# Optimization experiments

Measured on AMD Instinct MI355X. Metric: run time of the kernel, lower is better.

## Reference

```python
import jax, jax.numpy as jnp
import numpy as np

B, S, H, NH, G = 2, 2048, 2048, 16, 2
HD = H // NH          # head_dim = 128
NKV = NH // G         # kv heads = 8
EPS = 1e-6


def setup_inputs() -> dict:
    key = jax.random.key(0)
    ks = jax.random.split(key, 5)
    sc = 0.02
    return {
        "x": jax.random.normal(ks[0], (B, S, H), jnp.float32),
        "wq": jax.random.normal(ks[1], (H, H), jnp.float32) * sc,
        "wk": jax.random.normal(ks[2], (H, H // G), jnp.float32) * sc,
        "wv": jax.random.normal(ks[3], (H, H // G), jnp.float32) * sc,
        "wo": jax.random.normal(ks[4], (H, H), jnp.float32) * sc,
        "rms_w": jnp.ones((HD,), jnp.float32),
        "token_positions": jnp.arange(S, dtype=jnp.int32),
    }


def _rmsnorm(x, w):
    # x: (b, s, HD, n_heads); normalize over the head_dim axis (axis 2)
    ms = jnp.mean(x * x, axis=2, keepdims=True)
    return x * jax.lax.rsqrt(ms + EPS) * w[None, None, :, None]


def _rope(x, pos):
    # x: (b, s, HD, n); interleaved-pair rotation along HD, base 10000
    half = HD // 2
    inv_freq = 1.0 / (10000.0 ** (jnp.arange(half, dtype=jnp.float32) * 2.0 / HD))
    ang = pos.astype(jnp.float32)[:, None] * inv_freq[None, :]   # (s, HD/2)
    cos = jnp.cos(ang)[None, :, :, None]
    sin = jnp.sin(ang)[None, :, :, None]
    x1 = x[:, :, 0::2, :]
    x2 = x[:, :, 1::2, :]
    r1 = x1 * cos - x2 * sin
    r2 = x1 * sin + x2 * cos
    return jnp.stack([r1, r2], axis=3).reshape(x.shape)


def reference(x, wq, wk, wv, wo, rms_w, token_positions):
    b, s, _ = x.shape
    # projections, split hidden as (head_dim, n_heads) exactly like the torch .view
    q = (x @ wq).reshape(b, s, HD, NH)
    k = (x @ wk).reshape(b, s, HD, NKV)
    v = (x @ wv).reshape(b, s, HD, NKV)
    # per-head RMSNorm (over head_dim) then RoPE on Q and K
    q = _rope(_rmsnorm(q, rms_w), token_positions)
    k = _rope(_rmsnorm(k, rms_w), token_positions)
    # grouped-query attention: group G query heads per kv head
    q5 = q.reshape(b, s, HD, NKV, G)
    scores = jnp.einsum('bsdkg,btdk->bkgst', q5, k)          # (b,NKV,G,s,s)
    mask = jnp.triu(jnp.ones((s, s), bool), 1)               # causal
    scores = jnp.where(mask[None, None, None], -jnp.inf, scores)
    attn = jax.nn.softmax(scores / jnp.sqrt(jnp.float32(HD)), axis=-1)
    ctx = jnp.einsum('bkgst,btdk->bkgsd', attn, v)           # (b,NKV,G,s,HD)
    ctx = ctx.reshape(b, NH, s, HD).transpose(0, 2, 1, 3).reshape(b, s, H)
    return ctx @ wo
```

## Files before the change

kernel.cpp:

```cpp
#include <hip/hip_runtime.h>
#include <hip/hip_bf16.h>
#include <stdint.h>

typedef unsigned short u16;
typedef uint32_t u32;
typedef __attribute__((ext_vector_type(8))) short s8v;
typedef __attribute__((ext_vector_type(4))) float f4v;
typedef __attribute__((ext_vector_type(4))) unsigned int u4v;

#define SQ   2048
#define HDIM 2048
#define HD_  128
#define NH_  16
#define NKV_ 8

__device__ __forceinline__ u16 f2b(float f) {
  uint32_t u = __builtin_bit_cast(uint32_t, f);
  u += 0x7fffu + ((u >> 16) & 1u);
  return (u16)(u >> 16);
}
__device__ __forceinline__ float b2f(u16 v) {
  uint32_t u = ((uint32_t)v) << 16;
  return __builtin_bit_cast(float, u);
}
__device__ __forceinline__ u32 cvtpk(float lo, float hi) {
  u32 r;
  asm("v_cvt_pk_bf16_f32 %0, %1, %2" : "=v"(r) : "v"(lo), "v"(hi));
  return r;
}

__global__ __launch_bounds__(256) void k_prep(const float* __restrict__ x,
                                              const float* __restrict__ wq,
                                              const float* __restrict__ wk,
                                              const float* __restrict__ wv,
                                              const float* __restrict__ wo,
                                              u16* __restrict__ xb,
                                              u16* __restrict__ wqt,
                                              u16* __restrict__ wkt,
                                              u16* __restrict__ wvt,
                                              u16* __restrict__ wot) {
  const int z = blockIdx.z;
  if (z == 4) {
    size_t i = ((size_t)(blockIdx.y * 64 + blockIdx.x) * 256 + threadIdx.x) * 2;
#pragma unroll
    for (int j = 0; j < 2; j++) {
      f4v v = *(const f4v*)(x + (i + j) * 4);
      union { u16 s[4]; uint64_t u; } o;
      o.s[0] = f2b(v[0]); o.s[1] = f2b(v[1]); o.s[2] = f2b(v[2]); o.s[3] = f2b(v[3]);
      *(uint64_t*)(xb + (i + j) * 4) = o.u;
    }
    return;
  }
  const float* in = (z == 0) ? wq : (z == 1) ? wk : (z == 2) ? wv : wo;
  u16* out = (z == 0) ? wqt : (z == 1) ? wkt : (z == 2) ? wvt : wot;
  const int cols = (z == 1 || z == 2) ? 1024 : 2048;
  int c0 = blockIdx.x * 32, r0 = blockIdx.y * 32;
  if (c0 >= cols) return;
  __shared__ float tile[32][33];
  int tx = threadIdx.x & 31, ty = threadIdx.x >> 5;
#pragma unroll
  for (int i = 0; i < 32; i += 8)
    tile[ty + i][tx] = in[(size_t)(r0 + ty + i) * cols + c0 + tx];
  __syncthreads();
#pragma unroll
  for (int i = 0; i < 32; i += 8)
    out[(size_t)(c0 + ty + i) * 2048 + r0 + tx] = f2b(tile[tx][ty + i]);
}

template <int BN, int F32OUT>
__global__ __launch_bounds__(512, 2) void k_gemm256(const u16* __restrict__ A,
                                                    const u16* __restrict__ Bt,
                                                    void* __restrict__ C,
                                                    int M, int N, int K) {
  constexpr int NB = BN / 64;
  constexpr int NF = BN / 64;
  __shared__ __align__(16) u16 Al[2][256 * 64];
  __shared__ __align__(16) u16 Bl[2][BN * 64];
  const int tid = threadIdx.x;
  const int lane = tid & 63, wid = tid >> 6;
  const int wm = wid >> 2, wn = wid & 3;
  const int l15 = lane & 15, l4 = lane >> 4;
  const int m0 = blockIdx.y * 256, n0 = blockIdx.x * BN;
  auto* A3 = (__attribute__((address_space(3))) char*)&Al[0][0];
  auto* B3 = (__attribute__((address_space(3))) char*)&Bl[0][0];
  int srow[4], soff[4];
#pragma unroll
  for (int j = 0; j < 4; j++) {
    int slot = j * 8192 + tid * 16;
    srow[j] = slot >> 7;
    soff[j] = (((slot >> 4) & 7) ^ (srow[j] & 7)) * 16;
  }
  int xk2[2];
#pragma unroll
  for (int ks = 0; ks < 2; ks++) xk2[ks] = (((ks * 4 + l4) ^ (l15 & 7)) << 4);

#define STAGEAB(buf, k0s)                                                         \
  do {                                                                            \
    _Pragma("unroll")                                                             \
    for (int j = 0; j < 4; j++) {                                                 \
      const char* gA = (const char*)(A + (size_t)(m0 + srow[j]) * K + (k0s)) + soff[j]; \
      __builtin_amdgcn_global_load_lds(                                           \
          (const __attribute__((address_space(1))) void*)gA,                      \
          (__attribute__((address_space(3))) void*)(A3 + (buf) * 32768 + j * 8192 + tid * 16), \
          16, 0, 0);                                                              \
    }                                                                             \
    _Pragma("unroll")                                                             \
    for (int j = 0; j < NB; j++) {                                                \
      const char* gB = (const char*)(Bt + (size_t)(n0 + srow[j]) * K + (k0s)) + soff[j]; \
      __builtin_amdgcn_global_load_lds(                                           \
          (const __attribute__((address_space(1))) void*)gB,                      \
          (__attribute__((address_space(3))) void*)(B3 + (buf) * (BN * 128) + j * 8192 + tid * 16), \
          16, 0, 0);                                                              \
    }                                                                             \
  } while (0)

  f4v acc[8][NF] = {};
  STAGEAB(0, 0);
  STAGEAB(1, 64);
  const int nK = K >> 6;
  for (int t = 0; t < nK; t++) {
    if (t == nK - 1)  asm volatile("s_waitcnt vmcnt(0)" ::: "memory");
    else if (NB == 4) asm volatile("s_waitcnt vmcnt(8)" ::: "memory");
    else              asm volatile("s_waitcnt vmcnt(6)" ::: "memory");
    __builtin_amdgcn_s_barrier();
    __builtin_amdgcn_sched_barrier(0);
    const char* Ab = (const char*)&Al[0][0] + (t & 1) * 32768;
    const char* Bb = (const char*)&Bl[0][0] + (t & 1) * (BN * 128);
#pragma unroll
    for (int qm = 0; qm < 2; qm++)
#pragma unroll
      for (int qn = 0; qn < 2; qn++) {
        s8v af[4][2], bf2[NF / 2][2];
#pragma unroll
        for (int i2 = 0; i2 < 4; i2++) {
          int row = wm * 128 + (qm * 4 + i2) * 16 + l15;
#pragma unroll
          for (int ks = 0; ks < 2; ks++)
            af[i2][ks] = *(const s8v*)(Ab + row * 128 + xk2[ks]);
        }
#pragma unroll
        for (int j2 = 0; j2 < NF / 2; j2++) {
          int row = wn * (NF * 16) + (qn * (NF / 2) + j2) * 16 + l15;
#pragma unroll
          for (int ks = 0; ks < 2; ks++)
            bf2[j2][ks] = *(const s8v*)(Bb + row * 128 + xk2[ks]);
        }
        __builtin_amdgcn_s_setprio(1);
#pragma unroll
        for (int i2 = 0; i2 < 4; i2++)
#pragma unroll
          for (int j2 = 0; j2 < NF / 2; j2++)
#pragma unroll
            for (int ks = 0; ks < 2; ks++)
              acc[qm * 4 + i2][qn * (NF / 2) + j2] = __builtin_amdgcn_mfma_f32_16x16x32_bf16(
                  af[i2][ks], bf2[j2][ks], acc[qm * 4 + i2][qn * (NF / 2) + j2], 0, 0, 0);
        __builtin_amdgcn_s_setprio(0);
      }
    __builtin_amdgcn_sched_barrier(0);
    if (t + 2 < nK) {
      __builtin_amdgcn_s_barrier();
      STAGEAB(t & 1, (t + 2) * 64);
    }
  }
#undef STAGEAB
#pragma unroll
  for (int mi = 0; mi < 8; mi++)
#pragma unroll
    for (int ni = 0; ni < NF; ni++) {
      int mb = m0 + wm * 128 + mi * 16 + l4 * 4;
      int nn = n0 + wn * (NF * 16) + ni * 16 + l15;
#pragma unroll
      for (int r = 0; r < 4; r++) {
        float v = acc[mi][ni][r];
        if (F32OUT) ((float*)C)[(size_t)(mb + r) * N + nn] = v;
        else        ((u16*)C)[(size_t)(mb + r) * N + nn]  = f2b(v);
      }
    }
}

__global__ __launch_bounds__(256) void k_normrope(const u16* __restrict__ qkv,
                                                  const float* __restrict__ rms_w,
                                                  const int* __restrict__ pos_arr,
                                                  u16* __restrict__ qq,
                                                  u16* __restrict__ kko,
                                                  u16* __restrict__ vto) {
  int idx = blockIdx.x;
  int b = idx >> 11, s = idx & 2047;
  int t = threadIdx.x;
  __shared__ float part[256];
  __shared__ float rstdq[16], rstdk[8];
  __shared__ float lcos[64], lsin[64];
  float pos = (float)pos_arr[s];
  if (t < 64) {
    float ang = pos * exp2f(-0.20762050593046f * (float)t);
    float sn, cs;
    sincosf(ang, &sn, &cs);
    lcos[t] = cs; lsin[t] = sn;
  }
  const u16* qr = qkv + (size_t)idx * 4096;
  const u16* kr = qr + 2048;
  const u16* vr = qr + 3072;
  int h = t & 15, ch = t >> 4;
  float qv[8]; float ss = 0.f;
#pragma unroll
  for (int j = 0; j < 8; j++) {
    float v = b2f(qr[(ch * 8 + j) * 16 + h]);
    qv[j] = v; ss += v * v;
  }
  part[t] = ss;
  __syncthreads();
  if (t < 16) {
    float tot = 0.f;
#pragma unroll
    for (int c = 0; c < 16; c++) tot += part[c * 16 + t];
    rstdq[t] = rsqrtf(tot * (1.f / 128.f) + 1e-6f);
  }
  __syncthreads();
  {
    float rs = rstdq[h];
    s8v ov;
#pragma unroll
    for (int p = 0; p < 4; p++) {
      int d0 = ch * 8 + p * 2;
      float v0 = qv[p * 2]     * rs * rms_w[d0];
      float v1 = qv[p * 2 + 1] * rs * rms_w[d0 + 1];
      float cs = lcos[d0 >> 1], sn = lsin[d0 >> 1];
      ov[p * 2]     = (short)f2b((v0 * cs - v1 * sn) * 0.08838834764831845f);
      ov[p * 2 + 1] = (short)f2b((v0 * sn + v1 * cs) * 0.08838834764831845f);
    }
    *(s8v*)(qq + ((size_t)(b * 16 + h) * SQ + s) * HD_ + ch * 8) = ov;
  }
  __syncthreads();
  int kv = t & 7, ch2 = t >> 3;
  float kvs[8]; float ssk = 0.f;
  if (t < 128) {
#pragma unroll
    for (int j = 0; j < 8; j++) {
      float v = b2f(kr[(ch2 * 8 + j) * 8 + kv]);
      kvs[j] = v; ssk += v * v;
    }
    part[t] = ssk;
  }
  __syncthreads();
  if (t < 8) {
    float tot = 0.f;
#pragma unroll
    for (int c = 0; c < 16; c++) tot += part[c * 8 + t];
    rstdk[t] = rsqrtf(tot * (1.f / 128.f) + 1e-6f);
  }
  __syncthreads();
  if (t < 128) {
    float rs = rstdk[kv];
    s8v ov;
#pragma unroll
    for (int p = 0; p < 4; p++) {
      int d0 = ch2 * 8 + p * 2;
      float v0 = kvs[p * 2]     * rs * rms_w[d0];
      float v1 = kvs[p * 2 + 1] * rs * rms_w[d0 + 1];
      float cs = lcos[d0 >> 1], sn = lsin[d0 >> 1];
      ov[p * 2]     = (short)f2b(v0 * cs - v1 * sn);
      ov[p * 2 + 1] = (short)f2b(v0 * sn + v1 * cs);
    }
    *(s8v*)(kko + ((size_t)(b * 8 + kv) * SQ + s) * HD_ + ch2 * 8) = ov;
#pragma unroll
    for (int j = 0; j < 8; j++) {
      int d = ch2 * 8 + j;
      vto[((size_t)(b * 8 + kv) * HD_ + d) * SQ + s] = vr[d * 8 + kv];
    }
  }
}

__global__ __launch_bounds__(512, 2) void k_attn(const u16* __restrict__ qq,
                                                 const u16* __restrict__ kk,
                                                 const u16* __restrict__ vt,
                                                 u16* __restrict__ ctx) {
  const int tile = (blockIdx.z == 1) ? (15 - (int)blockIdx.x) : (int)blockIdx.x;
  const int s0 = tile * 128;
  const int h  = blockIdx.y;
  const int b  = blockIdx.z;
  const int kvh = h >> 1;
  const int tid = threadIdx.x, lane = tid & 63, w = tid >> 6;
  const int l15 = lane & 15, l4 = lane >> 4;
  __shared__ __align__(16) u16 Kl[2][64 * 128];
  __shared__ __align__(16) u16 Vl[2][128 * 64];
  auto* K3 = (__attribute__((address_space(3))) char*)&Kl[0][0];
  auto* V3 = (__attribute__((address_space(3))) char*)&Vl[0][0];
  const u16* qbase = qq + (size_t)(b * 16 + h) * SQ * HD_;
  const u16* kbase = kk + (size_t)(b * 8 + kvh) * SQ * HD_;
  const u16* vbase = vt + (size_t)(b * 8 + kvh) * HD_ * SQ;
  const int swp = s0 + w * 16;
  const int mybound = swp + 16;
  const int ntiles = 2 * tile + 2;

  int krow[2], kgo[2], vrow[2], vgo[2];
#pragma unroll
  for (int j = 0; j < 2; j++) {
    int s = j * 8192 + tid * 16;
    krow[j] = s >> 8;
    kgo[j]  = (((s >> 4) & 15) ^ (krow[j] & 7)) * 8;
    vrow[j] = s >> 7;
    vgo[j]  = (((s >> 4) & 7) ^ (vrow[j] & 7)) * 8;
  }

#define STAGE(buf, t0s)                                                           \
  do {                                                                            \
    _Pragma("unroll")                                                             \
    for (int j = 0; j < 2; j++) {                                                 \
      const u16* gk = kbase + (size_t)((t0s) + krow[j]) * HD_ + kgo[j];           \
      __builtin_amdgcn_global_load_lds(                                           \
          (const __attribute__((address_space(1))) void*)gk,                      \
          (__attribute__((address_space(3))) void*)(K3 + (buf) * 16384 + j * 8192 + tid * 16), \
          16, 0, 0);                                                              \
      const u16* gv = vbase + (size_t)vrow[j] * SQ + (t0s) + vgo[j];              \
      __builtin_amdgcn_global_load_lds(                                           \
          (const __attribute__((address_space(1))) void*)gv,                      \
          (__attribute__((address_space(3))) void*)(V3 + (buf) * 16384 + j * 8192 + tid * 16), \
          16, 0, 0);                                                              \
    }                                                                             \
  } while (0)

  s8v qf[4];
#pragma unroll
  for (int c = 0; c < 4; c++)
    qf[c] = *(const s8v*)(qbase + (size_t)(swp + l15) * HD_ + c * 32 + l4 * 8);

  f4v o[8] = {};
  float m2 = -1e30f, l2 = 0.f;

  const int src1 = ((l4 & 1) << 5) + l15;
  const int src2 = src1 + 16;
  const bool selhi = (l4 >> 1) != 0;
  const int swzk = (l15 & 7);

  int xk[4], xv[2];
#pragma unroll
  for (int c = 0; c < 4; c++) xk[c] = ((c * 4 + l4) ^ swzk) * 8;
#pragma unroll
  for (int ks = 0; ks < 2; ks++) xv[ks] = ((ks * 4 + l4) ^ swzk) * 8;

  STAGE(0, 0);
  STAGE(1, 64);
  int cur = 0;
  for (int i = 0; i < ntiles; i++) {
    const int t0 = i * 64;
    asm volatile("s_waitcnt vmcnt(4)" ::: "memory");
    __builtin_amdgcn_s_barrier();
    __builtin_amdgcn_sched_barrier(0);
    if (t0 < mybound) {
      const u16* kb = &Kl[cur][0];
      const u16* vb = &Vl[cur][0];
      f4v sc[4] = {};
      __builtin_amdgcn_s_setprio(1);
#pragma unroll
      for (int tt = 0; tt < 4; tt++) {
        s8v kf0 = *(const s8v*)(kb + (tt * 16 + l15) * 128 + xk[0]);
        s8v kf1 = *(const s8v*)(kb + (tt * 16 + l15) * 128 + xk[1]);
        s8v kf2 = *(const s8v*)(kb + (tt * 16 + l15) * 128 + xk[2]);
        s8v kf3 = *(const s8v*)(kb + (tt * 16 + l15) * 128 + xk[3]);
        sc[tt] = __builtin_amdgcn_mfma_f32_16x16x32_bf16(kf0, qf[0], sc[tt], 0, 0, 0);
        sc[tt] = __builtin_amdgcn_mfma_f32_16x16x32_bf16(kf1, qf[1], sc[tt], 0, 0, 0);
        sc[tt] = __builtin_amdgcn_mfma_f32_16x16x32_bf16(kf2, qf[2], sc[tt], 0, 0, 0);
        sc[tt] = __builtin_amdgcn_mfma_f32_16x16x32_bf16(kf3, qf[3], sc[tt], 0, 0, 0);
      }
      __builtin_amdgcn_s_setprio(0);
      if (t0 + 63 > swp) {
#pragma unroll
        for (int tt = 0; tt < 4; tt++)
#pragma unroll
          for (int r = 0; r < 4; r++) {
            int tg = t0 + tt * 16 + l4 * 4 + r;
            if (tg > swp + l15) sc[tt][r] = -1e30f;
          }
      }
      float mx = sc[0][0];
#pragma unroll
      for (int tt = 0; tt < 4; tt++)
#pragma unroll
        for (int r = 0; r < 4; r++) mx = fmaxf(mx, sc[tt][r]);
      mx = fmaxf(mx, __shfl_xor(mx, 16));
      mx = fmaxf(mx, __shfl_xor(mx, 32));
      if (__any(mx > m2 + 8.f)) {
        float mn = fmaxf(m2, mx);
        float sf = exp2f((m2 - mn) * 1.44269504f);
        m2 = mn; l2 *= sf;
#pragma unroll
        for (int dd = 0; dd < 8; dd++)
#pragma unroll
          for (int r = 0; r < 4; r++) o[dd][r] *= sf;
      }
      u32 pk[4][2];
      float sum = 0.f;
#pragma unroll
      for (int tt = 0; tt < 4; tt++) {
        float p0 = exp2f((sc[tt][0] - m2) * 1.44269504f);
        float p1 = exp2f((sc[tt][1] - m2) * 1.44269504f);
        float p2 = exp2f((sc[tt][2] - m2) * 1.44269504f);
        float p3 = exp2f((sc[tt][3] - m2) * 1.44269504f);
        sum += (p0 + p1) + (p2 + p3);
        pk[tt][0] = cvtpk(p0, p1);
        pk[tt][1] = cvtpk(p2, p3);
      }
      sum += __shfl_xor(sum, 16);
      sum += __shfl_xor(sum, 32);
      l2 += sum;
      s8v pf[2];
#pragma unroll
      for (int ks = 0; ks < 2; ks++) {
        u32 e00 = (u32)__shfl((int)pk[2 * ks][0], src1);
        u32 e01 = (u32)__shfl((int)pk[2 * ks][1], src1);
        u32 e10 = (u32)__shfl((int)pk[2 * ks + 1][0], src1);
        u32 e11 = (u32)__shfl((int)pk[2 * ks + 1][1], src1);
        u32 f00 = (u32)__shfl((int)pk[2 * ks][0], src2);
        u32 f01 = (u32)__shfl((int)pk[2 * ks][1], src2);
        u32 f10 = (u32)__shfl((int)pk[2 * ks + 1][0], src2);
        u32 f11 = (u32)__shfl((int)pk[2 * ks + 1][1], src2);
        u4v fr;
        fr[0] = selhi ? e10 : e00;
        fr[1] = selhi ? e11 : e01;
        fr[2] = selhi ? f10 : f00;
        fr[3] = selhi ? f11 : f01;
        pf[ks] = __builtin_bit_cast(s8v, fr);
      }
      __builtin_amdgcn_s_setprio(1);
#pragma unroll
      for (int dd = 0; dd < 8; dd++) {
        s8v vf0 = *(const s8v*)(vb + (dd * 16 + l15) * 64 + xv[0]);
        s8v vf1 = *(const s8v*)(vb + (dd * 16 + l15) * 64 + xv[1]);
        o[dd] = __builtin_amdgcn_mfma_f32_16x16x32_bf16(vf0, pf[0], o[dd], 0, 0, 0);
        o[dd] = __builtin_amdgcn_mfma_f32_16x16x32_bf16(vf1, pf[1], o[dd], 0, 0, 0);
      }
      __builtin_amdgcn_s_setprio(0);
    }
    __builtin_amdgcn_sched_barrier(0);
    __builtin_amdgcn_s_barrier();
    if (i + 2 < ntiles) STAGE(cur, t0 + 128);
    cur ^= 1;
  }
#undef STAGE
  float inv = 1.f / l2;
  size_t rowoff = ((size_t)(b * SQ + swp + l15)) * HDIM + h * HD_;
#pragma unroll
  for (int dd = 0; dd < 8; dd++) {
    *(u32*)(ctx + rowoff + dd * 16 + l4 * 4)     = cvtpk(o[dd][0] * inv, o[dd][1] * inv);
    *(u32*)(ctx + rowoff + dd * 16 + l4 * 4 + 2) = cvtpk(o[dd][2] * inv, o[dd][3] * inv);
  }
}

extern "C" void kernel_launch(void* const* d_in, const int* in_sizes, int n_in,
                              void* d_out, int out_size, void* d_ws, size_t ws_size,
                              hipStream_t stream) {
  const float* x     = (const float*)d_in[0];
  const float* wq    = (const float*)d_in[1];
  const float* wk    = (const float*)d_in[2];
  const float* wv    = (const float*)d_in[3];
  const float* wo    = (const float*)d_in[4];
  const float* rms_w = (const float*)d_in[5];
  const int*   pos   = (const int*)d_in[6];

  u16* w = (u16*)d_ws;
  u16* xb   = w;
  u16* wqt  = xb   + 8388608;
  u16* wkt  = wqt  + 4194304;
  u16* wvt  = wkt  + 2097152;
  u16* wot  = wvt  + 2097152;
  u16* qkvraw = wot + 4194304;
  u16* kkb  = qkvraw + 16777216;
  u16* vtb  = kkb  + 4194304;
  u16* qqb  = wqt;
  u16* ctxb = xb;

  k_prep<<<dim3(64, 64, 5), 256, 0, stream>>>(x, wq, wk, wv, wo, xb, wqt, wkt, wvt, wot);

  k_gemm256<256, 0><<<dim3(16, 16), 512, 0, stream>>>(xb, wqt, qkvraw, 4096, 4096, 2048);

  k_normrope<<<4096, 256, 0, stream>>>(qkvraw, rms_w, pos, qqb, kkb, vtb);

  k_attn<<<dim3(16, 16, 2), 512, 0, stream>>>(qqb, kkb, vtb, ctxb);

  k_gemm256<128, 1><<<dim3(16, 16), 512, 0, stream>>>(ctxb, wot, d_out, 4096, 2048, 2048);
}
```

Measured before the change: 263.8 us.

## Give each attention wave two query row groups and swap output GEMM for 128x128 kernel

The attention kernel now runs 4 waves per block, each handling 32 query rows (two 16-row groups). Each K/V fragment read from LDS is reused for two MFMA groups, which halves LDS traffic per FLOP at the cost of more registers and fewer waves to hide latency. The output projection moves from the double-buffered 256-row GEMM to a new single-buffered 128x128 tile GEMM with more blocks. That GEMM has no load/compute overlap, and its scalar fp32 stores may be less efficient.

Measured after the change: 261.5 us. No clear change (-0.9%).

```diff
diff --git a/kernel.cpp b/kernel.cpp
--- a/kernel.cpp
+++ b/kernel.cpp
@@ -65,6 +65,78 @@
 #pragma unroll
   for (int i = 0; i < 32; i += 8)
     out[(size_t)(c0 + ty + i) * 2048 + r0 + tx] = f2b(tile[tx][ty + i]);
+}
+
+template <int F32OUT>
+__global__ __launch_bounds__(256) void k_gemm(const u16* __restrict__ A,
+                                              const u16* __restrict__ Bt,
+                                              void* __restrict__ C,
+                                              int M, int N, int K) {
+  __shared__ __align__(16) u16 As[128 * 64];
+  __shared__ __align__(16) u16 Bs[128 * 64];
+  const int tid = threadIdx.x;
+  const int lane = tid & 63, wvi = tid >> 6;
+  const int wm = wvi >> 1, wn = wvi & 1;
+  const int l15 = lane & 15, l4 = lane >> 4;
+  const int m0 = blockIdx.y * 128, n0 = blockIdx.x * 128;
+  auto* As3 = (__attribute__((address_space(3))) char*)As;
+  auto* Bs3 = (__attribute__((address_space(3))) char*)Bs;
+  int srow[4], soff[4];
+#pragma unroll
+  for (int i = 0; i < 4; i++) {
+    int slot = wvi * 4096 + i * 1024 + lane * 16;
+    int r = slot >> 7;
+    int gc = ((slot >> 4) & 7) ^ (r & 7);
+    srow[i] = r; soff[i] = gc * 16;
+  }
+  f4v acc[4][4] = {};
+  for (int k0 = 0; k0 < K; k0 += 64) {
+#pragma unroll
+    for (int i = 0; i < 4; i++) {
+      const char* gA = (const char*)(A + (size_t)(m0 + srow[i]) * K + k0) + soff[i];
+      const char* gB = (const char*)(Bt + (size_t)(n0 + srow[i]) * K + k0) + soff[i];
+      __builtin_amdgcn_global_load_lds((__attribute__((address_space(1))) void*)gA,
+                                       (__attribute__((address_space(3))) void*)(As3 + wvi * 4096 + i * 1024),
+                                       16, 0, 0);
+      __builtin_amdgcn_global_load_lds((__attribute__((address_space(1))) void*)gB,
+                                       (__attribute__((address_space(3))) void*)(Bs3 + wvi * 4096 + i * 1024),
+                                       16, 0, 0);
+    }
+    __syncthreads();
+#pragma unroll
+    for (int kk = 0; kk < 2; kk++) {
+      s8v af[4], bf[4];
+#pragma unroll
+      for (int i = 0; i < 4; i++) {
+        int ra = wm * 64 + i * 16 + l15;
+        af[i] = *(const s8v*)((const char*)As + ra * 128 +
+                              ((kk * 64 + l4 * 16) ^ ((ra & 7) << 4)));
+        int rb = wn * 64 + i * 16 + l15;
+        bf[i] = *(const s8v*)((const char*)Bs + rb * 128 +
+                              ((kk * 64 + l4 * 16) ^ ((rb & 7) << 4)));
+      }
+#pragma unroll
+      for (int i = 0; i < 4; i++)
+#pragma unroll
+        for (int j = 0; j < 4; j++)
+          acc[i][j] = __builtin_amdgcn_mfma_f32_16x16x32_bf16(af[i], bf[j], acc[i][j], 0, 0, 0);
+    }
+    __syncthreads();
+  }
+#pragma unroll
+  for (int i = 0; i < 4; i++) {
+#pragma unroll
+    for (int j = 0; j < 4; j++) {
+      int mb = m0 + wm * 64 + i * 16 + l4 * 4;
+      int nn = n0 + wn * 64 + j * 16 + l15;
+#pragma unroll
+      for (int r = 0; r < 4; r++) {
+        float v = acc[i][j][r];
+        if (F32OUT) ((float*)C)[(size_t)(mb + r) * N + nn] = v;
+        else        ((u16*)C)[(size_t)(mb + r) * N + nn]  = f2b(v);
+      }
+    }
+  }
 }
 
 template <int BN, int F32OUT>
@@ -270,7 +342,7 @@
   }
 }
 
-__global__ __launch_bounds__(512, 2) void k_attn(const u16* __restrict__ qq,
+__global__ __launch_bounds__(256, 2) void k_attn(const u16* __restrict__ qq,
                                                  const u16* __restrict__ kk,
                                                  const u16* __restrict__ vt,
                                                  u16* __restrict__ ctx) {
@@ -288,14 +360,14 @@
   const u16* qbase = qq + (size_t)(b * 16 + h) * SQ * HD_;
   const u16* kbase = kk + (size_t)(b * 8 + kvh) * SQ * HD_;
   const u16* vbase = vt + (size_t)(b * 8 + kvh) * HD_ * SQ;
-  const int swp = s0 + w * 16;
-  const int mybound = swp + 16;
+  const int swp = s0 + w * 32;
+  const int mybound = swp + 32;
   const int ntiles = 2 * tile + 2;
 
-  int krow[2], kgo[2], vrow[2], vgo[2];
-#pragma unroll
-  for (int j = 0; j < 2; j++) {
-    int s = j * 8192 + tid * 16;
+  int krow[4], kgo[4], vrow[4], vgo[4];
+#pragma unroll
+  for (int j = 0; j < 4; j++) {
+    int s = j * 4096 + tid * 16;
     krow[j] = s >> 8;
     kgo[j]  = (((s >> 4) & 15) ^ (krow[j] & 7)) * 8;
     vrow[j] = s >> 7;
@@ -305,27 +377,30 @@
 #define STAGE(buf, t0s)                                                           \
   do {                                                                            \
     _Pragma("unroll")                                                             \
-    for (int j = 0; j < 2; j++) {                                                 \
+    for (int j = 0; j < 4; j++) {                                                 \
       const u16* gk = kbase + (size_t)((t0s) + krow[j]) * HD_ + kgo[j];           \
       __builtin_amdgcn_global_load_lds(                                           \
           (const __attribute__((address_space(1))) void*)gk,                      \
-          (__attribute__((address_space(3))) void*)(K3 + (buf) * 16384 + j * 8192 + tid * 16), \
+          (__attribute__((address_space(3))) void*)(K3 + (buf) * 16384 + j * 4096 + tid * 16), \
           16, 0, 0);                                                              \
       const u16* gv = vbase + (size_t)vrow[j] * SQ + (t0s) + vgo[j];              \
       __builtin_amdgcn_global_load_lds(                                           \
           (const __attribute__((address_space(1))) void*)gv,                      \
-          (__attribute__((address_space(3))) void*)(V3 + (buf) * 16384 + j * 8192 + tid * 16), \
+          (__attribute__((address_space(3))) void*)(V3 + (buf) * 16384 + j * 4096 + tid * 16), \
           16, 0, 0);                                                              \
     }                                                                             \
   } while (0)
 
-  s8v qf[4];
-#pragma unroll
-  for (int c = 0; c < 4; c++)
-    qf[c] = *(const s8v*)(qbase + (size_t)(swp + l15) * HD_ + c * 32 + l4 * 8);
-
-  f4v o[8] = {};
-  float m2 = -1e30f, l2 = 0.f;
+  s8v qf[2][4];
+#pragma unroll
+  for (int g = 0; g < 2; g++)
+#pragma unroll
+    for (int c = 0; c < 4; c++)
+      qf[g][c] = *(const s8v*)(qbase + (size_t)(swp + g * 16 + l15) * HD_ + c * 32 + l4 * 8);
+
+  f4v o[2][8] = {};
+  float m2[2] = {-1e30f, -1e30f};
+  float l2[2] = {0.f, 0.f};
 
   const int src1 = ((l4 & 1) << 5) + l15;
   const int src2 = src1 + 16;
@@ -343,13 +418,14 @@
   int cur = 0;
   for (int i = 0; i < ntiles; i++) {
     const int t0 = i * 64;
-    asm volatile("s_waitcnt vmcnt(4)" ::: "memory");
+    if (i == ntiles - 1) asm volatile("s_waitcnt vmcnt(0)" ::: "memory");
+    else                 asm volatile("s_waitcnt vmcnt(8)" ::: "memory");
     __builtin_amdgcn_s_barrier();
     __builtin_amdgcn_sched_barrier(0);
     if (t0 < mybound) {
       const u16* kb = &Kl[cur][0];
       const u16* vb = &Vl[cur][0];
-      f4v sc[4] = {};
+      f4v sc[4][2] = {};
       __builtin_amdgcn_s_setprio(1);
 #pragma unroll
       for (int tt = 0; tt < 4; tt++) {
@@ -357,77 +433,89 @@
         s8v kf1 = *(const s8v*)(kb + (tt * 16 + l15) * 128 + xk[1]);
         s8v kf2 = *(const s8v*)(kb + (tt * 16 + l15) * 128 + xk[2]);
         s8v kf3 = *(const s8v*)(kb + (tt * 16 + l15) * 128 + xk[3]);
-        sc[tt] = __builtin_amdgcn_mfma_f32_16x16x32_bf16(kf0, qf[0], sc[tt], 0, 0, 0);
-        sc[tt] = __builtin_amdgcn_mfma_f32_16x16x32_bf16(kf1, qf[1], sc[tt], 0, 0, 0);
-        sc[tt] = __builtin_amdgcn_mfma_f32_16x16x32_bf16(kf2, qf[2], sc[tt], 0, 0, 0);
-        sc[tt] = __builtin_amdgcn_mfma_f32_16x16x32_bf16(kf3, qf[3], sc[tt], 0, 0, 0);
+        sc[tt][0] = __builtin_amdgcn_mfma_f32_16x16x32_bf16(kf0, qf[0][0], sc[tt][0], 0, 0, 0);
+        sc[tt][0] = __builtin_amdgcn_mfma_f32_16x16x32_bf16(kf1, qf[0][1], sc[tt][0], 0, 0, 0);
+        sc[tt][0] = __builtin_amdgcn_mfma_f32_16x16x32_bf16(kf2, qf[0][2], sc[tt][0], 0, 0, 0);
+        sc[tt][0] = __builtin_amdgcn_mfma_f32_16x16x32_bf16(kf3, qf[0][3], sc[tt][0], 0, 0, 0);
+        sc[tt][1] = __builtin_amdgcn_mfma_f32_16x16x32_bf16(kf0, qf[1][0], sc[tt][1], 0, 0, 0);
+        sc[tt][1] = __builtin_amdgcn_mfma_f32_16x16x32_bf16(kf1, qf[1][1], sc[tt][1], 0, 0, 0);
+        sc[tt][1] = __builtin_amdgcn_mfma_f32_16x16x32_bf16(kf2, qf[1][2], sc[tt][1], 0, 0, 0);
+        sc[tt][1] = __builtin_amdgcn_mfma_f32_16x16x32_bf16(kf3, qf[1][3], sc[tt][1], 0, 0, 0);
       }
       __builtin_amdgcn_s_setprio(0);
       if (t0 + 63 > swp) {
 #pragma unroll
         for (int tt = 0; tt < 4; tt++)
 #pragma unroll
-          for (int r = 0; r < 4; r++) {
-            int tg = t0 + tt * 16 + l4 * 4 + r;
-            if (tg > swp + l15) sc[tt][r] = -1e30f;
-          }
-      }
-      float mx = sc[0][0];
-#pragma unroll
-      for (int tt = 0; tt < 4; tt++)
-#pragma unroll
-        for (int r = 0; r < 4; r++) mx = fmaxf(mx, sc[tt][r]);
-      mx = fmaxf(mx, __shfl_xor(mx, 16));
-      mx = fmaxf(mx, __shfl_xor(mx, 32));
-      if (__any(mx > m2 + 8.f)) {
-        float mn = fmaxf(m2, mx);
-        float sf = exp2f((m2 - mn) * 1.44269504f);
-        m2 = mn; l2 *= sf;
-#pragma unroll
-        for (int dd = 0; dd < 8; dd++)
-#pragma unroll
-          for (int r = 0; r < 4; r++) o[dd][r] *= sf;
-      }
-      u32 pk[4][2];
-      float sum = 0.f;
-#pragma unroll
-      for (int tt = 0; tt < 4; tt++) {
-        float p0 = exp2f((sc[tt][0] - m2) * 1.44269504f);
-        float p1 = exp2f((sc[tt][1] - m2) * 1.44269504f);
-        float p2 = exp2f((sc[tt][2] - m2) * 1.44269504f);
-        float p3 = exp2f((sc[tt][3] - m2) * 1.44269504f);
-        sum += (p0 + p1) + (p2 + p3);
-        pk[tt][0] = cvtpk(p0, p1);
-        pk[tt][1] = cvtpk(p2, p3);
-      }
-      sum += __shfl_xor(sum, 16);
-      sum += __shfl_xor(sum, 32);
-      l2 += sum;
-      s8v pf[2];
-#pragma unroll
-      for (int ks = 0; ks < 2; ks++) {
-        u32 e00 = (u32)__shfl((int)pk[2 * ks][0], src1);
-        u32 e01 = (u32)__shfl((int)pk[2 * ks][1], src1);
-        u32 e10 = (u32)__shfl((int)pk[2 * ks + 1][0], src1);
-        u32 e11 = (u32)__shfl((int)pk[2 * ks + 1][1], src1);
-        u32 f00 = (u32)__shfl((int)pk[2 * ks][0], src2);
-        u32 f01 = (u32)__shfl((int)pk[2 * ks][1], src2);
-        u32 f10 = (u32)__shfl((int)pk[2 * ks + 1][0], src2);
-        u32 f11 = (u32)__shfl((int)pk[2 * ks + 1][1], src2);
-        u4v fr;
-        fr[0] = selhi ? e10 : e00;
-        fr[1] = selhi ? e11 : e01;
-        fr[2] = selhi ? f10 : f00;
-        fr[3] = selhi ? f11 : f01;
-        pf[ks] = __builtin_bit_cast(s8v, fr);
+          for (int g = 0; g < 2; g++)
+#pragma unroll
+            for (int r = 0; r < 4; r++) {
+              int tg = t0 + tt * 16 + l4 * 4 + r;
+              int sg = swp + g * 16 + l15;
+              if (tg > sg) sc[tt][g][r] = -1e30f;
+            }
+      }
+      s8v pf[2][2];
+#pragma unroll
+      for (int g = 0; g < 2; g++) {
+        float mx = sc[0][g][0];
+#pragma unroll
+        for (int tt = 0; tt < 4; tt++)
+#pragma unroll
+          for (int r = 0; r < 4; r++) mx = fmaxf(mx, sc[tt][g][r]);
+        mx = fmaxf(mx, __shfl_xor(mx, 16));
+        mx = fmaxf(mx, __shfl_xor(mx, 32));
+        if (__any(mx > m2[g] + 8.f)) {
+          float mn = fmaxf(m2[g], mx);
+          float sf = exp2f((m2[g] - mn) * 1.44269504f);
+          m2[g] = mn; l2[g] *= sf;
+#pragma unroll
+          for (int dd = 0; dd < 8; dd++)
+#pragma unroll
+            for (int r = 0; r < 4; r++) o[g][dd][r] *= sf;
+        }
+        u32 pk[4][2];
+        float sum = 0.f;
+#pragma unroll
+        for (int tt = 0; tt < 4; tt++) {
+          float p0 = exp2f((sc[tt][g][0] - m2[g]) * 1.44269504f);
+          float p1 = exp2f((sc[tt][g][1] - m2[g]) * 1.44269504f);
+          float p2 = exp2f((sc[tt][g][2] - m2[g]) * 1.44269504f);
+          float p3 = exp2f((sc[tt][g][3] - m2[g]) * 1.44269504f);
+          sum += (p0 + p1) + (p2 + p3);
+          pk[tt][0] = cvtpk(p0, p1);
+          pk[tt][1] = cvtpk(p2, p3);
+        }
+        sum += __shfl_xor(sum, 16);
+        sum += __shfl_xor(sum, 32);
+        l2[g] += sum;
+#pragma unroll
+        for (int ks = 0; ks < 2; ks++) {
+          u32 e00 = (u32)__shfl((int)pk[2 * ks][0], src1);
+          u32 e01 = (u32)__shfl((int)pk[2 * ks][1], src1);
+          u32 e10 = (u32)__shfl((int)pk[2 * ks + 1][0], src1);
+          u32 e11 = (u32)__shfl((int)pk[2 * ks + 1][1], src1);
+          u32 f00 = (u32)__shfl((int)pk[2 * ks][0], src2);
+          u32 f01 = (u32)__shfl((int)pk[2 * ks][1], src2);
+          u32 f10 = (u32)__shfl((int)pk[2 * ks + 1][0], src2);
+          u32 f11 = (u32)__shfl((int)pk[2 * ks + 1][1], src2);
+          u4v fr;
+          fr[0] = selhi ? e10 : e00;
+          fr[1] = selhi ? e11 : e01;
+          fr[2] = selhi ? f10 : f00;
+          fr[3] = selhi ? f11 : f01;
+          pf[g][ks] = __builtin_bit_cast(s8v, fr);
+        }
       }
       __builtin_amdgcn_s_setprio(1);
 #pragma unroll
       for (int dd = 0; dd < 8; dd++) {
         s8v vf0 = *(const s8v*)(vb + (dd * 16 + l15) * 64 + xv[0]);
         s8v vf1 = *(const s8v*)(vb + (dd * 16 + l15) * 64 + xv[1]);
-        o[dd] = __builtin_amdgcn_mfma_f32_16x16x32_bf16(vf0, pf[0], o[dd], 0, 0, 0);
-        o[dd] = __builtin_amdgcn_mfma_f32_16x16x32_bf16(vf1, pf[1], o[dd], 0, 0, 0);
+        o[0][dd] = __builtin_amdgcn_mfma_f32_16x16x32_bf16(vf0, pf[0][0], o[0][dd], 0, 0, 0);
+        o[0][dd] = __builtin_amdgcn_mfma_f32_16x16x32_bf16(vf1, pf[0][1], o[0][dd], 0, 0, 0);
+        o[1][dd] = __builtin_amdgcn_mfma_f32_16x16x32_bf16(vf0, pf[1][0], o[1][dd], 0, 0, 0);
+        o[1][dd] = __builtin_amdgcn_mfma_f32_16x16x32_bf16(vf1, pf[1][1], o[1][dd], 0, 0, 0);
       }
       __builtin_amdgcn_s_setprio(0);
     }
@@ -437,12 +525,15 @@
     cur ^= 1;
   }
 #undef STAGE
-  float inv = 1.f / l2;
-  size_t rowoff = ((size_t)(b * SQ + swp + l15)) * HDIM + h * HD_;
-#pragma unroll
-  for (int dd = 0; dd < 8; dd++) {
-    *(u32*)(ctx + rowoff + dd * 16 + l4 * 4)     = cvtpk(o[dd][0] * inv, o[dd][1] * inv);
-    *(u32*)(ctx + rowoff + dd * 16 + l4 * 4 + 2) = cvtpk(o[dd][2] * inv, o[dd][3] * inv);
+#pragma unroll
+  for (int g = 0; g < 2; g++) {
+    float inv = 1.f / l2[g];
+    size_t rowoff = ((size_t)(b * SQ + swp + g * 16 + l15)) * HDIM + h * HD_;
+#pragma unroll
+    for (int dd = 0; dd < 8; dd++) {
+      *(u32*)(ctx + rowoff + dd * 16 + l4 * 4)     = cvtpk(o[g][dd][0] * inv, o[g][dd][1] * inv);
+      *(u32*)(ctx + rowoff + dd * 16 + l4 * 4 + 2) = cvtpk(o[g][dd][2] * inv, o[g][dd][3] * inv);
+    }
   }
 }
 
@@ -475,7 +566,7 @@
 
   k_normrope<<<4096, 256, 0, stream>>>(qkvraw, rms_w, pos, qqb, kkb, vtb);
 
-  k_attn<<<dim3(16, 16, 2), 512, 0, stream>>>(qqb, kkb, vtb, ctxb);
-
-  k_gemm256<128, 1><<<dim3(16, 16), 512, 0, stream>>>(ctxb, wot, d_out, 4096, 2048, 2048);
-}
+  k_attn<<<dim3(16, 16, 2), 256, 0, stream>>>(qqb, kkb, vtb, ctxb);
+
+  k_gemm<1><<<dim3(16, 32), 256, 0, stream>>>(ctxb, wot, d_out, 4096, 2048, 2048);
+}
```
